# Kernel tuning notes

Measured on AMD Instinct MI355X. Metric: run time of the kernel, lower is better.

## Reference

```python
import jax, jax.numpy as jnp
import numpy as np

N = 100000          # num nodes
D_IN = 256          # input feature dim
D_OUT = 64          # per-head output dim
N_HEADS = 4
MOTIF_POSITIONS = (2, 3)   # positions per motif (2 motifs, 5 total positions)
P_TOTAL = 5
E = 3_200_000       # edges per motif-position adjacency (avg degree 32)


def setup_inputs() -> dict:
    key = jax.random.key(0)
    ks = jax.random.split(key, 7)
    x = jax.random.normal(ks[0], (D_IN, N), jnp.float32)
    # glorot-ish scales
    shrink_mats = jax.random.normal(ks[1], (2, N_HEADS, D_OUT, D_IN), jnp.float32) * 0.08
    att0 = jax.random.normal(ks[2], (P_TOTAL, N_HEADS, D_OUT), jnp.float32) * 0.17
    att1 = jax.random.normal(ks[3], (P_TOTAL, N_HEADS, D_OUT), jnp.float32) * 0.17
    edge_rows = jax.random.randint(ks[4], (P_TOTAL, E), 0, N, jnp.int32)
    edge_cols = jax.random.randint(ks[5], (P_TOTAL, E), 0, N, jnp.int32)
    edge_vals = jax.random.uniform(ks[6], (P_TOTAL, E), jnp.float32)
    return dict(x=x, shrink_mats=shrink_mats, att0=att0, att1=att1,
                edge_rows=edge_rows, edge_cols=edge_cols, edge_vals=edge_vals)


def reference(x, shrink_mats, att0, att1, edge_rows, edge_cols, edge_vals):
    # x: [D_IN, N]; shrink_mats: [M, H, D_OUT, D_IN]; att0/att1: [P_TOTAL, H, D_OUT]
    # edge_rows/cols/vals: [P_TOTAL, E] sparse adjacency per motif-position.
    offsets = (0, MOTIF_POSITIONS[0])
    motif_outs = []
    for m, P in enumerate(MOTIF_POSITIONS):
        head_outs = []
        for i in range(N_HEADS):
            h = (shrink_mats[m, i] @ x).T            # [N, D_OUT] node features per head
            acc = jnp.zeros((N, D_OUT), x.dtype)
            for k in range(P):
                p = offsets[m] + k
                r, c, v = edge_rows[p], edge_cols[p], edge_vals[p]
                a0 = h @ att0[p, i]                  # [N] col-side score
                a1 = h @ att1[p, i]                  # [N] row-side score
                s = v * (a0[c] + a1[r])              # edge scores = adj * (att0[j] + att1[i])
                smax = jax.ops.segment_max(s, r, num_segments=N)
                e = jnp.exp(s - smax[r])             # stable row-wise sparse softmax
                den = jax.ops.segment_sum(e, r, num_segments=N)
                w = e / den[r]                       # [E] attention weights
                acc = acc + jax.ops.segment_sum(w[:, None] * h[c], r, num_segments=N)
            head_outs.append(jax.nn.elu(acc.T))      # [D_OUT, N]
        motif_outs.append(jnp.concatenate(head_outs, axis=0))  # [H*D_OUT, N]
    # original returns a list (one per motif); all shapes match so stack them
    return jnp.stack(motif_outs, axis=0)             # [M, H*D_OUT, N]
```

## Files before the change

kernel.cpp:

```cpp
#include <hip/hip_runtime.h>
#include <hip/hip_bf16.h>
#include <math.h>

#define N_NODES 100000
#define D_IN 256
#define D_OUT 64
#define N_HEADS 4
#define P_TOTAL 5
#define NEDGE 3200000

__device__ __forceinline__ unsigned short f2bf(float f) {
    unsigned u = __float_as_uint(f);
    unsigned r = (u + 0x7FFFu + ((u >> 16) & 1u)) >> 16;
    return (unsigned short)r;
}

__global__ void zero_kernel(int* __restrict__ p, int n) {
    int i = blockIdx.x * blockDim.x + threadIdx.x;
    if (i < n) p[i] = 0;
}

__global__ __launch_bounds__(256)
void gemm_h(const float* __restrict__ x, const float* __restrict__ W,
            const float* __restrict__ att0, const float* __restrict__ att1,
            unsigned short* __restrict__ Hb,
            float* __restrict__ A0, float* __restrict__ A1) {
    const int m  = blockIdx.z;
    const int i  = blockIdx.y;
    const int c0 = i * 64;
    const int n0 = blockIdx.x * 128;
    __shared__ float xs[32][132];
    __shared__ float ws[32][68];
    const int t  = threadIdx.x;
    const int c4 = (t & 15) * 4;
    const int n8 = (t >> 4) * 8;
    float acc[8][4];
#pragma unroll
    for (int a = 0; a < 8; ++a)
#pragma unroll
        for (int b = 0; b < 4; ++b) acc[a][b] = 0.f;

    for (int k0 = 0; k0 < 256; k0 += 32) {
#pragma unroll
        for (int it = 0; it < 16; ++it) {
            int idx = it * 256 + t;
            int kk = idx >> 7;
            int nn = idx & 127;
            int gn = n0 + nn;
            xs[kk][nn] = (gn < N_NODES) ? x[(size_t)(k0 + kk) * N_NODES + gn] : 0.f;
        }
#pragma unroll
        for (int it = 0; it < 8; ++it) {
            int idx = it * 256 + t;
            int cc = idx >> 5;
            int kk = idx & 31;
            ws[kk][cc] = W[((size_t)(m * 256 + c0 + cc)) * 256 + (k0 + kk)];
        }
        __syncthreads();
#pragma unroll
        for (int k = 0; k < 32; ++k) {
            float4 wv  = *(const float4*)&ws[k][c4];
            float4 xv0 = *(const float4*)&xs[k][n8];
            float4 xv1 = *(const float4*)&xs[k][n8 + 4];
            float xa[8] = {xv0.x, xv0.y, xv0.z, xv0.w, xv1.x, xv1.y, xv1.z, xv1.w};
            float wa[4] = {wv.x, wv.y, wv.z, wv.w};
#pragma unroll
            for (int a = 0; a < 8; ++a)
#pragma unroll
                for (int b = 0; b < 4; ++b) acc[a][b] += xa[a] * wa[b];
        }
        __syncthreads();
    }
#pragma unroll
    for (int a = 0; a < 8; ++a) {
        int gn = n0 + n8 + a;
        if (gn < N_NODES) {
            ushort4 s4;
            s4.x = f2bf(acc[a][0]); s4.y = f2bf(acc[a][1]);
            s4.z = f2bf(acc[a][2]); s4.w = f2bf(acc[a][3]);
            *(ushort4*)&Hb[((size_t)m * N_NODES + gn) * 256 + c0 + c4] = s4;
        }
    }
    const int p0 = m ? 2 : 0;
    const int np = m ? 3 : 2;
    for (int pk = 0; pk < np; ++pk) {
        const int pi = (p0 + pk) * 4 + i;
        float a0v[4], a1v[4];
#pragma unroll
        for (int b = 0; b < 4; ++b) {
            a0v[b] = att0[pi * 64 + c4 + b];
            a1v[b] = att1[pi * 64 + c4 + b];
        }
#pragma unroll
        for (int a = 0; a < 8; ++a) {
            float s0 = 0.f, s1 = 0.f;
#pragma unroll
            for (int b = 0; b < 4; ++b) {
                s0 += acc[a][b] * a0v[b];
                s1 += acc[a][b] * a1v[b];
            }
#pragma unroll
            for (int off = 1; off < 16; off <<= 1) {
                s0 += __shfl_xor(s0, off);
                s1 += __shfl_xor(s1, off);
            }
            int gn = n0 + n8 + a;
            if ((t & 15) == 0 && gn < N_NODES) {
                A0[(size_t)pi * N_NODES + gn] = s0;
                A1[(size_t)pi * N_NODES + gn] = s1;
            }
        }
    }
}

__global__ __launch_bounds__(256)
void hist_kernel(const int* __restrict__ rows, int* __restrict__ counts) {
    const int p = blockIdx.y;
    const int e = blockIdx.x * 256 + threadIdx.x;
    int r = rows[(size_t)p * NEDGE + e];
    atomicAdd(&counts[p * N_NODES + r], 1);
}

__global__ __launch_bounds__(1024)
void scan1(const int* __restrict__ counts, int* __restrict__ rowstart,
           int* __restrict__ blocksum) {
    __shared__ int sh[1024];
    const int p = blockIdx.y, b = blockIdx.x, t = threadIdx.x;
    const int i = b * 1024 + t;
    int v = (i < N_NODES) ? counts[p * N_NODES + i] : 0;
    sh[t] = v;
    __syncthreads();
    for (int off = 1; off < 1024; off <<= 1) {
        int y = (t >= off) ? sh[t - off] : 0;
        __syncthreads();
        sh[t] += y;
        __syncthreads();
    }
    if (i < N_NODES) rowstart[p * (N_NODES + 1) + i] = sh[t] - v;
    if (t == 1023) blocksum[p * 128 + b] = sh[t];
}

__global__ __launch_bounds__(128)
void scan2(int* __restrict__ blocksum, int* __restrict__ rowstart, int nb) {
    __shared__ int sh[128];
    const int p = blockIdx.x, t = threadIdx.x;
    int v = (t < nb) ? blocksum[p * 128 + t] : 0;
    sh[t] = v;
    __syncthreads();
    for (int off = 1; off < 128; off <<= 1) {
        int y = (t >= off) ? sh[t - off] : 0;
        __syncthreads();
        sh[t] += y;
        __syncthreads();
    }
    blocksum[p * 128 + t] = sh[t] - v;
    if (t == 0) rowstart[p * (N_NODES + 1) + N_NODES] = NEDGE;
}

__global__ __launch_bounds__(1024)
void scan3(int* __restrict__ rowstart, const int* __restrict__ blocksum) {
    const int p = blockIdx.y, b = blockIdx.x, t = threadIdx.x;
    const int i = b * 1024 + t;
    if (i < N_NODES) rowstart[p * (N_NODES + 1) + i] += blocksum[p * 128 + b];
}

__global__ __launch_bounds__(256)
void scatter_kernel(const int* __restrict__ rows, const int* __restrict__ cols,
                    const float* __restrict__ vals, const int* __restrict__ rowstart,
                    int* __restrict__ cursor, unsigned* __restrict__ cv) {
    const int p = blockIdx.y;
    const size_t base = (size_t)p * NEDGE;
    const size_t e = (size_t)blockIdx.x * 256 + threadIdx.x;
    int r = rows[base + e];
    int c = cols[base + e];
    float v = vals[base + e];
    int q = (int)(v * 32768.0f + 0.5f);
    if (q > 32767) q = 32767;
    unsigned cu = ((unsigned)c << 15) | (unsigned)q;
    int pos = rowstart[p * (N_NODES + 1) + r] + atomicAdd(&cursor[p * N_NODES + r], 1);
    cv[base + pos] = cu;
}

__global__ __launch_bounds__(256)
void row_pass(const unsigned short* __restrict__ Hb, const float* __restrict__ A0,
              const float* __restrict__ A1, const int* __restrict__ rowstart,
              const unsigned* __restrict__ cv, float* __restrict__ out) {
    const int m  = blockIdx.y;
    const int r0 = blockIdx.x * 16;
    const int w  = threadIdx.x >> 6;
    const int l  = threadIdx.x & 63;
    const int head = l >> 4;
    const int hN = head * N_NODES;
    __shared__ float tile[16][260];
    const int p0 = m ? 2 : 0;
    const int np = m ? 3 : 2;
    const unsigned long long* Hm64 =
        (const unsigned long long*)(Hb + (size_t)m * N_NODES * 256);

    for (int rt = 0; rt < 4; ++rt) {
        const int r = r0 + w * 4 + rt;
        float acc0 = 0.f, acc1 = 0.f, acc2 = 0.f, acc3 = 0.f;
        for (int pk = 0; pk < np; ++pk) {
            const int p = p0 + pk;
            const int* rs = rowstart + p * (N_NODES + 1);
            const int e0 = __builtin_amdgcn_readfirstlane(rs[r]);
            const int e1 = __builtin_amdgcn_readfirstlane(rs[r + 1]);
            if (e1 <= e0) continue;
            const float a1r = A1[(size_t)(p * 4) * N_NODES + hN + r];
            const float* A0p = A0 + (size_t)(p * 4) * N_NODES;
            const unsigned* cvp = cv + (size_t)p * NEDGE;
            float den = 0.f;
            float num0 = 0.f, num1 = 0.f, num2 = 0.f, num3 = 0.f;
            int e = e0;
            const int e1m = e0 + ((e1 - e0) & ~3);
            for (; e < e1m; e += 4) {
                unsigned cu0 = cvp[e + 0];
                unsigned cu1 = cvp[e + 1];
                unsigned cu2 = cvp[e + 2];
                unsigned cu3 = cvp[e + 3];
                int c0 = (int)(cu0 >> 15);
                int c1 = (int)(cu1 >> 15);
                int c2 = (int)(cu2 >> 15);
                int c3 = (int)(cu3 >> 15);
                float a00 = A0p[hN + c0];
                float a01 = A0p[hN + c1];
                float a02 = A0p[hN + c2];
                float a03 = A0p[hN + c3];
                const unsigned long long* h0p = Hm64 + (size_t)c0 * 64;
                const unsigned long long* h1p = Hm64 + (size_t)c1 * 64;
                const unsigned long long* h2p = Hm64 + (size_t)c2 * 64;
                const unsigned long long* h3p = Hm64 + (size_t)c3 * 64;
                unsigned long long hv0 = h0p[l];
                unsigned long long hv1 = h1p[l];
                unsigned long long hv2 = h2p[l];
                unsigned long long hv3 = h3p[l];
                float w0 = __expf((float)(cu0 & 32767u) * (1.0f / 32768.0f) * (a00 + a1r));
                float w1 = __expf((float)(cu1 & 32767u) * (1.0f / 32768.0f) * (a01 + a1r));
                float w2 = __expf((float)(cu2 & 32767u) * (1.0f / 32768.0f) * (a02 + a1r));
                float w3 = __expf((float)(cu3 & 32767u) * (1.0f / 32768.0f) * (a03 + a1r));
                den += w0 + w1 + w2 + w3;
                {
                    unsigned lo = (unsigned)hv0, hi = (unsigned)(hv0 >> 32);
                    num0 += w0 * __uint_as_float(lo << 16);
                    num1 += w0 * __uint_as_float(lo & 0xFFFF0000u);
                    num2 += w0 * __uint_as_float(hi << 16);
                    num3 += w0 * __uint_as_float(hi & 0xFFFF0000u);
                }
                {
                    unsigned lo = (unsigned)hv1, hi = (unsigned)(hv1 >> 32);
                    num0 += w1 * __uint_as_float(lo << 16);
                    num1 += w1 * __uint_as_float(lo & 0xFFFF0000u);
                    num2 += w1 * __uint_as_float(hi << 16);
                    num3 += w1 * __uint_as_float(hi & 0xFFFF0000u);
                }
                {
                    unsigned lo = (unsigned)hv2, hi = (unsigned)(hv2 >> 32);
                    num0 += w2 * __uint_as_float(lo << 16);
                    num1 += w2 * __uint_as_float(lo & 0xFFFF0000u);
                    num2 += w2 * __uint_as_float(hi << 16);
                    num3 += w2 * __uint_as_float(hi & 0xFFFF0000u);
                }
                {
                    unsigned lo = (unsigned)hv3, hi = (unsigned)(hv3 >> 32);
                    num0 += w3 * __uint_as_float(lo << 16);
                    num1 += w3 * __uint_as_float(lo & 0xFFFF0000u);
                    num2 += w3 * __uint_as_float(hi << 16);
                    num3 += w3 * __uint_as_float(hi & 0xFFFF0000u);
                }
            }
            for (; e < e1; ++e) {
                unsigned cu = cvp[e];
                int c = (int)(cu >> 15);
                float a0v = A0p[hN + c];
                const unsigned long long* hp = Hm64 + (size_t)c * 64;
                unsigned long long hv = hp[l];
                float wv = __expf((float)(cu & 32767u) * (1.0f / 32768.0f) * (a0v + a1r));
                unsigned lo = (unsigned)hv, hi = (unsigned)(hv >> 32);
                den  += wv;
                num0 += wv * __uint_as_float(lo << 16);
                num1 += wv * __uint_as_float(lo & 0xFFFF0000u);
                num2 += wv * __uint_as_float(hi << 16);
                num3 += wv * __uint_as_float(hi & 0xFFFF0000u);
            }
            float rd = 1.0f / den;
            acc0 += num0 * rd;
            acc1 += num1 * rd;
            acc2 += num2 * rd;
            acc3 += num3 * rd;
        }
        acc0 = acc0 > 0.f ? acc0 : __expf(acc0) - 1.f;
        acc1 = acc1 > 0.f ? acc1 : __expf(acc1) - 1.f;
        acc2 = acc2 > 0.f ? acc2 : __expf(acc2) - 1.f;
        acc3 = acc3 > 0.f ? acc3 : __expf(acc3) - 1.f;
        *(float4*)&tile[w * 4 + rt][l * 4] = make_float4(acc0, acc1, acc2, acc3);
    }
    __syncthreads();
    {
        const int ch = threadIdx.x;
        float* dst = out + ((size_t)m * 256 + ch) * N_NODES + r0;
#pragma unroll
        for (int q = 0; q < 4; ++q) {
            float4 v4 = make_float4(tile[q * 4 + 0][ch], tile[q * 4 + 1][ch],
                                    tile[q * 4 + 2][ch], tile[q * 4 + 3][ch]);
            *(float4*)(dst + q * 4) = v4;
        }
    }
}

extern "C" void kernel_launch(void* const* d_in, const int* in_sizes, int n_in,
                              void* d_out, int out_size, void* d_ws, size_t ws_size,
                              hipStream_t stream) {
    const float* x    = (const float*)d_in[0];
    const float* W    = (const float*)d_in[1];
    const float* att0 = (const float*)d_in[2];
    const float* att1 = (const float*)d_in[3];
    const int*   erows = (const int*)d_in[4];
    const int*   ecols = (const int*)d_in[5];
    const float* evals = (const float*)d_in[6];
    float* out = (float*)d_out;

    char* ws = (char*)d_ws;
    size_t off = 0;
    auto alloc = [&](size_t bytes) -> void* {
        void* p = ws + off;
        off += (bytes + 255) & ~(size_t)255;
        return p;
    };
    unsigned short* Hb = (unsigned short*)alloc((size_t)2 * N_NODES * 256 * 2);
    float* A0       = (float*)alloc((size_t)P_TOTAL * N_HEADS * N_NODES * 4);
    float* A1       = (float*)alloc((size_t)P_TOTAL * N_HEADS * N_NODES * 4);
    int*   counts   = (int*)alloc((size_t)P_TOTAL * N_NODES * 4);
    int*   cursor   = (int*)alloc((size_t)P_TOTAL * N_NODES * 4);
    int*   rowstart = (int*)alloc((size_t)P_TOTAL * (N_NODES + 1) * 4);
    int*   blocksum = (int*)alloc((size_t)P_TOTAL * 128 * 4);
    unsigned* cv    = (unsigned*)alloc((size_t)P_TOTAL * NEDGE * 4);
    (void)ws_size; (void)in_sizes; (void)n_in; (void)out_size;

    const int nb = (N_NODES + 1023) / 1024;

    {
        int zn = P_TOTAL * N_NODES;
        zero_kernel<<<(zn + 1023) / 1024, 1024, 0, stream>>>(counts, zn);
        zero_kernel<<<(zn + 1023) / 1024, 1024, 0, stream>>>(cursor, zn);
    }
    gemm_h<<<dim3((N_NODES + 127) / 128, 4, 2), 256, 0, stream>>>(x, W, att0, att1, Hb, A0, A1);
    hist_kernel<<<dim3(NEDGE / 256, P_TOTAL), 256, 0, stream>>>(erows, counts);
    scan1<<<dim3(nb, P_TOTAL), 1024, 0, stream>>>(counts, rowstart, blocksum);
    scan2<<<P_TOTAL, 128, 0, stream>>>(blocksum, rowstart, nb);
    scan3<<<dim3(nb, P_TOTAL), 1024, 0, stream>>>(rowstart, blocksum);
    scatter_kernel<<<dim3(NEDGE / 256, P_TOTAL), 256, 0, stream>>>(erows, ecols, evals,
                                                                   rowstart, cursor, cv);
    row_pass<<<dim3(N_NODES / 16, 2), 256, 0, stream>>>(Hb, A0, A1, rowstart, cv, out);
}
```

Before: 3.876 ms.

## Split each wavefront into two half-waves gathering alternate edges with 16-byte loads

In the row pass, each lane now loads eight bf16 channels (a uint4) per neighbor instead of four. The two 32-lane halves of the wavefront handle alternating edges and are combined with a cross-half shuffle reduction before normalisation. This doubles the bytes per gather instruction and halves the number of sequential gather iterations per row, aiming to improve memory-level parallelism in the latency-bound gather. The cost is an extra shuffle reduction per position, more registers, and more tail-handling code.

```diff
diff --git a/kernel.cpp b/kernel.cpp
--- a/kernel.cpp
+++ b/kernel.cpp
@@ -14,6 +14,9 @@
     unsigned r = (u + 0x7FFFu + ((u >> 16) & 1u)) >> 16;
     return (unsigned short)r;
 }
+
+__device__ __forceinline__ float bfLO(unsigned u) { return __uint_as_float(u << 16); }
+__device__ __forceinline__ float bfHI(unsigned u) { return __uint_as_float(u & 0xFFFF0000u); }
 
 __global__ void zero_kernel(int* __restrict__ p, int n) {
     int i = blockIdx.x * blockDim.x + threadIdx.x;
@@ -185,21 +188,24 @@
 void row_pass(const unsigned short* __restrict__ Hb, const float* __restrict__ A0,
               const float* __restrict__ A1, const int* __restrict__ rowstart,
               const unsigned* __restrict__ cv, float* __restrict__ out) {
-    const int m  = blockIdx.y;
-    const int r0 = blockIdx.x * 16;
-    const int w  = threadIdx.x >> 6;
-    const int l  = threadIdx.x & 63;
-    const int head = l >> 4;
-    const int hN = head * N_NODES;
+    const int m    = blockIdx.y;
+    const int r0   = blockIdx.x * 16;
+    const int w    = threadIdx.x >> 6;
+    const int l    = threadIdx.x & 63;
+    const int half = l >> 5;
+    const int q    = l & 31;
+    const int head = q >> 3;
+    const int hN   = head * N_NODES;
+    const int ch0  = q * 8;
     __shared__ float tile[16][260];
     const int p0 = m ? 2 : 0;
     const int np = m ? 3 : 2;
-    const unsigned long long* Hm64 =
-        (const unsigned long long*)(Hb + (size_t)m * N_NODES * 256);
+    const uint4* Hm4 = (const uint4*)(Hb + (size_t)m * N_NODES * 256);
 
     for (int rt = 0; rt < 4; ++rt) {
         const int r = r0 + w * 4 + rt;
         float acc0 = 0.f, acc1 = 0.f, acc2 = 0.f, acc3 = 0.f;
+        float acc4 = 0.f, acc5 = 0.f, acc6 = 0.f, acc7 = 0.f;
         for (int pk = 0; pk < np; ++pk) {
             const int p = p0 + pk;
             const int* rs = rowstart + p * (N_NODES + 1);
@@ -211,98 +217,129 @@
             const unsigned* cvp = cv + (size_t)p * NEDGE;
             float den = 0.f;
             float num0 = 0.f, num1 = 0.f, num2 = 0.f, num3 = 0.f;
+            float num4 = 0.f, num5 = 0.f, num6 = 0.f, num7 = 0.f;
             int e = e0;
-            const int e1m = e0 + ((e1 - e0) & ~3);
-            for (; e < e1m; e += 4) {
-                unsigned cu0 = cvp[e + 0];
-                unsigned cu1 = cvp[e + 1];
-                unsigned cu2 = cvp[e + 2];
-                unsigned cu3 = cvp[e + 3];
-                int c0 = (int)(cu0 >> 15);
-                int c1 = (int)(cu1 >> 15);
-                int c2 = (int)(cu2 >> 15);
-                int c3 = (int)(cu3 >> 15);
-                float a00 = A0p[hN + c0];
-                float a01 = A0p[hN + c1];
-                float a02 = A0p[hN + c2];
-                float a03 = A0p[hN + c3];
-                const unsigned long long* h0p = Hm64 + (size_t)c0 * 64;
-                const unsigned long long* h1p = Hm64 + (size_t)c1 * 64;
-                const unsigned long long* h2p = Hm64 + (size_t)c2 * 64;
-                const unsigned long long* h3p = Hm64 + (size_t)c3 * 64;
-                unsigned long long hv0 = h0p[l];
-                unsigned long long hv1 = h1p[l];
-                unsigned long long hv2 = h2p[l];
-                unsigned long long hv3 = h3p[l];
-                float w0 = __expf((float)(cu0 & 32767u) * (1.0f / 32768.0f) * (a00 + a1r));
-                float w1 = __expf((float)(cu1 & 32767u) * (1.0f / 32768.0f) * (a01 + a1r));
-                float w2 = __expf((float)(cu2 & 32767u) * (1.0f / 32768.0f) * (a02 + a1r));
-                float w3 = __expf((float)(cu3 & 32767u) * (1.0f / 32768.0f) * (a03 + a1r));
-                den += w0 + w1 + w2 + w3;
-                {
-                    unsigned lo = (unsigned)hv0, hi = (unsigned)(hv0 >> 32);
-                    num0 += w0 * __uint_as_float(lo << 16);
-                    num1 += w0 * __uint_as_float(lo & 0xFFFF0000u);
-                    num2 += w0 * __uint_as_float(hi << 16);
-                    num3 += w0 * __uint_as_float(hi & 0xFFFF0000u);
-                }
-                {
-                    unsigned lo = (unsigned)hv1, hi = (unsigned)(hv1 >> 32);
-                    num0 += w1 * __uint_as_float(lo << 16);
-                    num1 += w1 * __uint_as_float(lo & 0xFFFF0000u);
-                    num2 += w1 * __uint_as_float(hi << 16);
-                    num3 += w1 * __uint_as_float(hi & 0xFFFF0000u);
-                }
-                {
-                    unsigned lo = (unsigned)hv2, hi = (unsigned)(hv2 >> 32);
-                    num0 += w2 * __uint_as_float(lo << 16);
-                    num1 += w2 * __uint_as_float(lo & 0xFFFF0000u);
-                    num2 += w2 * __uint_as_float(hi << 16);
-                    num3 += w2 * __uint_as_float(hi & 0xFFFF0000u);
-                }
-                {
-                    unsigned lo = (unsigned)hv3, hi = (unsigned)(hv3 >> 32);
-                    num0 += w3 * __uint_as_float(lo << 16);
-                    num1 += w3 * __uint_as_float(lo & 0xFFFF0000u);
-                    num2 += w3 * __uint_as_float(hi << 16);
-                    num3 += w3 * __uint_as_float(hi & 0xFFFF0000u);
-                }
-            }
-            for (; e < e1; ++e) {
-                unsigned cu = cvp[e];
-                int c = (int)(cu >> 15);
-                float a0v = A0p[hN + c];
-                const unsigned long long* hp = Hm64 + (size_t)c * 64;
-                unsigned long long hv = hp[l];
-                float wv = __expf((float)(cu & 32767u) * (1.0f / 32768.0f) * (a0v + a1r));
-                unsigned lo = (unsigned)hv, hi = (unsigned)(hv >> 32);
-                den  += wv;
-                num0 += wv * __uint_as_float(lo << 16);
-                num1 += wv * __uint_as_float(lo & 0xFFFF0000u);
-                num2 += wv * __uint_as_float(hi << 16);
-                num3 += wv * __uint_as_float(hi & 0xFFFF0000u);
-            }
+
+#define ACC8(WK, H4)                                   \
+    do {                                               \
+        num0 += (WK) * bfLO((H4).x);                   \
+        num1 += (WK) * bfHI((H4).x);                   \
+        num2 += (WK) * bfLO((H4).y);                   \
+        num3 += (WK) * bfHI((H4).y);                   \
+        num4 += (WK) * bfLO((H4).z);                   \
+        num5 += (WK) * bfHI((H4).z);                   \
+        num6 += (WK) * bfLO((H4).w);                   \
+        num7 += (WK) * bfHI((H4).w);                   \
+    } while (0)
+
+            for (; e + 8 <= e1; e += 8) {
+                unsigned cs0 = cvp[e + 0], cs1 = cvp[e + 1];
+                unsigned cs2 = cvp[e + 2], cs3 = cvp[e + 3];
+                unsigned cs4 = cvp[e + 4], cs5 = cvp[e + 5];
+                unsigned cs6 = cvp[e + 6], cs7 = cvp[e + 7];
+                unsigned cua = half ? cs1 : cs0;
+                unsigned cub = half ? cs3 : cs2;
+                unsigned cuc = half ? cs5 : cs4;
+                unsigned cud = half ? cs7 : cs6;
+                unsigned ca = cua >> 15, cb = cub >> 15, cc = cuc >> 15, cd = cud >> 15;
+                float a0a = A0p[hN + (int)ca];
+                float a0b = A0p[hN + (int)cb];
+                float a0c = A0p[hN + (int)cc];
+                float a0d = A0p[hN + (int)cd];
+                uint4 ha = Hm4[(size_t)ca * 32 + q];
+                uint4 hb = Hm4[(size_t)cb * 32 + q];
+                uint4 hc = Hm4[(size_t)cc * 32 + q];
+                uint4 hd = Hm4[(size_t)cd * 32 + q];
+                float wa = __expf((float)(cua & 32767u) * (1.0f / 32768.0f) * (a0a + a1r));
+                float wb = __expf((float)(cub & 32767u) * (1.0f / 32768.0f) * (a0b + a1r));
+                float wc = __expf((float)(cuc & 32767u) * (1.0f / 32768.0f) * (a0c + a1r));
+                float wd = __expf((float)(cud & 32767u) * (1.0f / 32768.0f) * (a0d + a1r));
+                den += wa + wb + wc + wd;
+                ACC8(wa, ha);
+                ACC8(wb, hb);
+                ACC8(wc, hc);
+                ACC8(wd, hd);
+            }
+            if (e + 4 <= e1) {
+                unsigned cs0 = cvp[e + 0], cs1 = cvp[e + 1];
+                unsigned cs2 = cvp[e + 2], cs3 = cvp[e + 3];
+                unsigned cua = half ? cs1 : cs0;
+                unsigned cub = half ? cs3 : cs2;
+                unsigned ca = cua >> 15, cb = cub >> 15;
+                float a0a = A0p[hN + (int)ca];
+                float a0b = A0p[hN + (int)cb];
+                uint4 ha = Hm4[(size_t)ca * 32 + q];
+                uint4 hb = Hm4[(size_t)cb * 32 + q];
+                float wa = __expf((float)(cua & 32767u) * (1.0f / 32768.0f) * (a0a + a1r));
+                float wb = __expf((float)(cub & 32767u) * (1.0f / 32768.0f) * (a0b + a1r));
+                den += wa + wb;
+                ACC8(wa, ha);
+                ACC8(wb, hb);
+                e += 4;
+            }
+            if (e + 2 <= e1) {
+                unsigned cs0 = cvp[e + 0], cs1 = cvp[e + 1];
+                unsigned cua = half ? cs1 : cs0;
+                unsigned ca = cua >> 15;
+                float a0a = A0p[hN + (int)ca];
+                uint4 ha = Hm4[(size_t)ca * 32 + q];
+                float wa = __expf((float)(cua & 32767u) * (1.0f / 32768.0f) * (a0a + a1r));
+                den += wa;
+                ACC8(wa, ha);
+                e += 2;
+            }
+            if (e < e1) {
+                unsigned cua = cvp[e];
+                unsigned ca = cua >> 15;
+                float a0a = A0p[hN + (int)ca];
+                uint4 ha = Hm4[(size_t)ca * 32 + q];
+                float wa = __expf((float)(cua & 32767u) * (1.0f / 32768.0f) * (a0a + a1r));
+                wa = half ? 0.f : wa;
+                den += wa;
+                ACC8(wa, ha);
+            }
+#undef ACC8
+            den  += __shfl_xor(den, 32);
+            num0 += __shfl_xor(num0, 32);
+            num1 += __shfl_xor(num1, 32);
+            num2 += __shfl_xor(num2, 32);
+            num3 += __shfl_xor(num3, 32);
+            num4 += __shfl_xor(num4, 32);
+            num5 += __shfl_xor(num5, 32);
+            num6 += __shfl_xor(num6, 32);
+            num7 += __shfl_xor(num7, 32);
             float rd = 1.0f / den;
             acc0 += num0 * rd;
             acc1 += num1 * rd;
             acc2 += num2 * rd;
             acc3 += num3 * rd;
+            acc4 += num4 * rd;
+            acc5 += num5 * rd;
+            acc6 += num6 * rd;
+            acc7 += num7 * rd;
         }
         acc0 = acc0 > 0.f ? acc0 : __expf(acc0) - 1.f;
         acc1 = acc1 > 0.f ? acc1 : __expf(acc1) - 1.f;
         acc2 = acc2 > 0.f ? acc2 : __expf(acc2) - 1.f;
         acc3 = acc3 > 0.f ? acc3 : __expf(acc3) - 1.f;
-        *(float4*)&tile[w * 4 + rt][l * 4] = make_float4(acc0, acc1, acc2, acc3);
+        acc4 = acc4 > 0.f ? acc4 : __expf(acc4) - 1.f;
+        acc5 = acc5 > 0.f ? acc5 : __expf(acc5) - 1.f;
+        acc6 = acc6 > 0.f ? acc6 : __expf(acc6) - 1.f;
+        acc7 = acc7 > 0.f ? acc7 : __expf(acc7) - 1.f;
+        if (half == 0) {
+            *(float4*)&tile[w * 4 + rt][ch0]     = make_float4(acc0, acc1, acc2, acc3);
+            *(float4*)&tile[w * 4 + rt][ch0 + 4] = make_float4(acc4, acc5, acc6, acc7);
+        }
     }
     __syncthreads();
     {
         const int ch = threadIdx.x;
         float* dst = out + ((size_t)m * 256 + ch) * N_NODES + r0;
 #pragma unroll
-        for (int q = 0; q < 4; ++q) {
-            float4 v4 = make_float4(tile[q * 4 + 0][ch], tile[q * 4 + 1][ch],
-                                    tile[q * 4 + 2][ch], tile[q * 4 + 3][ch]);
-            *(float4*)(dst + q * 4) = v4;
+        for (int t4 = 0; t4 < 4; ++t4) {
+            float4 v4 = make_float4(tile[t4 * 4 + 0][ch], tile[t4 * 4 + 1][ch],
+                                    tile[t4 * 4 + 2][ch], tile[t4 * 4 + 3][ch]);
+            *(float4*)(dst + t4 * 4) = v4;
         }
     }
 }
```

Measured after the change: 3.858 ms. Within noise of the previous version (-0.5%).
